# Kernel optimization log

Hardware: AMD Instinct MI355X
Metric: run time of the kernel (lower is better)

## Reference

```python
import jax, jax.numpy as jnp
import numpy as np

N_HEADS = 2


def setup_inputs() -> dict:
    key = jax.random.key(0)
    ks = jax.random.split(key, 12)
    B, S, d, g = 4096, 32, 512, 512
    sp = (1.0 / np.sqrt(d))
    sg = (1.0 / np.sqrt(g))
    return {
        "source": jax.random.normal(ks[0], (B, d), jnp.float32),
        "gene": jax.random.normal(ks[1], (B, S, g), jnp.float32),
        "neighbors_padding_mask": jax.random.bernoulli(ks[2], 0.3, (B, S)),
        "mask_n": jax.random.uniform(ks[3], (B, 1), jnp.float32),
        "Wq": jax.random.normal(ks[4], (d, d), jnp.float32) * sp,
        "bq": jax.random.normal(ks[5], (d,), jnp.float32) * 0.02,
        "Wk": jax.random.normal(ks[6], (d, g), jnp.float32) * sg,
        "bk": jax.random.normal(ks[7], (d,), jnp.float32) * 0.02,
        "Wv": jax.random.normal(ks[8], (d, g), jnp.float32) * sg,
        "bv": jax.random.normal(ks[9], (d,), jnp.float32) * 0.02,
        "Wout": jax.random.normal(ks[10], (d, d), jnp.float32) * sp,
        "bout": jax.random.normal(ks[11], (d,), jnp.float32) * 0.02,
    }


def reference(source, gene, neighbors_padding_mask, mask_n,
              Wq, bq, Wk, bk, Wv, bv, Wout, bout):
    # attention_node.forward: 1-query masked MHA over S temporal neighbors.
    B, S, _ = gene.shape
    d = source.shape[1]
    H = N_HEADS
    hd = d // H

    # rows where every neighbor is padded -> unmask slot 0 (torch in-place fix)
    invalid = jnp.all(neighbors_padding_mask, axis=1, keepdims=True)      # [B,1]
    mask = neighbors_padding_mask.at[:, 0].set(
        jnp.where(invalid[:, 0], False, neighbors_padding_mask[:, 0]))

    # separate q/k/v projections (kdim=vdim=n_gene != embed_dim)
    q = (source @ Wq.T + bq) * (hd ** -0.5)                               # [B,d]
    k = gene @ Wk.T + bk                                                  # [B,S,d]
    v = gene @ Wv.T + bv                                                  # [B,S,d]

    qh = q.reshape(B, H, hd)
    kh = k.reshape(B, S, H, hd)
    vh = v.reshape(B, S, H, hd)

    scores = jnp.einsum('bhd,bshd->bhs', qh, kh)                          # [B,H,S]
    scores = jnp.where(mask[:, None, :], -jnp.inf, scores)
    w = jax.nn.softmax(scores, axis=-1)                                   # [B,H,S]

    attn = jnp.einsum('bhs,bshd->bhd', w, vh).reshape(B, d)               # [B,d]
    attn_out = attn @ Wout.T + bout

    # zero rows with no valid neighbors, gate, residual
    attn_out = jnp.where(invalid, jnp.float32(0), attn_out)
    out = attn_out * mask_n + source                                      # [B,d]
    attn_weight = w.mean(axis=1)                                          # avg over heads, [B,S]
    return out, attn_weight
```

## Files before the change

### kernel.cpp

```cpp
#include <hip/hip_runtime.h>
#include <hip/hip_bf16.h>
#include <math.h>
#include <stdint.h>


#define NB 4096
#define SNB 32
#define DM 512

typedef __attribute__((ext_vector_type(8))) short bf16x8;
typedef __attribute__((ext_vector_type(4))) float f32x4;

__device__ __forceinline__ unsigned short f2bf(float f) {
    union { float f; unsigned int u; } v; v.f = f;
    unsigned int u = v.u;
    return (unsigned short)((u + 0x7FFFu + ((u >> 16) & 1u)) >> 16);
}
__device__ __forceinline__ float bf2f(unsigned short s) {
    union { unsigned int u; float f; } v; v.u = ((unsigned int)s) << 16;
    return v.f;
}

__global__ void k_detect(const unsigned int* __restrict__ m, int* __restrict__ mode) {
    __shared__ int fF, fH;
    if (threadIdx.x == 0) { fF = 0; fH = 0; }
    __syncthreads();
    int lf = 0, lh = 0;
    for (int i = threadIdx.x; i < 32768; i += blockDim.x) {
        unsigned int w = m[i];
        lf |= (w == 0x3F800000u);
        lh |= ((w & 0xFFFFFF00u) != 0u);
    }
    if (lf) atomicOr(&fF, 1);
    if (lh) atomicOr(&fH, 1);
    __syncthreads();
    if (threadIdx.x == 0) *mode = fF ? 2 : (fH ? 1 : 0);
}

__global__ void k_conv_src(const float* __restrict__ s, unsigned short* __restrict__ d) {
    int i = blockIdx.x * 256 + threadIdx.x;
    float4 v = ((const float4*)s)[i];
    ushort4 o;
    o.x = f2bf(v.x); o.y = f2bf(v.y); o.z = f2bf(v.z); o.w = f2bf(v.w);
    ((ushort4*)d)[i] = o;
}

__global__ __launch_bounds__(256) void k_precomp_cd(
    const float* __restrict__ Wq, const float* __restrict__ Wk,
    const float* __restrict__ Wv, const float* __restrict__ Wout,
    unsigned short* __restrict__ C, unsigned short* __restrict__ D)
{
    __shared__ float Aa[32][33];
    __shared__ float Bb[32][33];
    int bid = blockIdx.x;
    int t = threadIdx.x;
    float acc0 = 0.f, acc1 = 0.f, acc2 = 0.f, acc3 = 0.f;

    if (bid < 512) {
        int h = bid >> 8, rem = bid & 255;
        int j0 = (rem >> 4) << 5, m0 = (rem & 15) << 5;
        int ml = t & 31, jg = (t >> 5) << 2;
        for (int ic = 0; ic < 8; ic++) {
            int ib = h * 256 + ic * 32;
            for (int q = 0; q < 4; q++) {
                int idx = t + q * 256, rr = idx >> 5, cc = idx & 31;
                Aa[rr][cc] = Wk[(size_t)(ib + rr) * 512 + j0 + cc];
                Bb[rr][cc] = Wq[(size_t)(ib + rr) * 512 + m0 + cc];
            }
            __syncthreads();
            for (int i = 0; i < 32; i++) {
                float bqv = Bb[i][ml];
                acc0 += Aa[i][jg + 0] * bqv;
                acc1 += Aa[i][jg + 1] * bqv;
                acc2 += Aa[i][jg + 2] * bqv;
                acc3 += Aa[i][jg + 3] * bqv;
            }
            __syncthreads();
        }
        size_t p = (size_t)h * 512 + j0 + jg;
        C[(p + 0) * 512 + m0 + ml] = f2bf(0.0625f * acc0);
        C[(p + 1) * 512 + m0 + ml] = f2bf(0.0625f * acc1);
        C[(p + 2) * 512 + m0 + ml] = f2bf(0.0625f * acc2);
        C[(p + 3) * 512 + m0 + ml] = f2bf(0.0625f * acc3);
    } else {
        int bid2 = bid - 512;
        int h = bid2 >> 8, rem = bid2 & 255;
        int n0 = (rem >> 4) << 5, j0 = (rem & 15) << 5;
        int jl = t & 31, ng = (t >> 5) << 2;
        for (int ic = 0; ic < 8; ic++) {
            int ib = h * 256 + ic * 32;
            for (int q = 0; q < 4; q++) {
                int idx = t + q * 256, rr = idx >> 5, cc = idx & 31;
                Aa[rr][cc] = Wout[(size_t)(n0 + rr) * 512 + ib + cc];
                Bb[rr][cc] = Wv[(size_t)(ib + rr) * 512 + j0 + cc];
            }
            __syncthreads();
            for (int i = 0; i < 32; i++) {
                float bvv = Bb[i][jl];
                acc0 += Aa[ng + 0][i] * bvv;
                acc1 += Aa[ng + 1][i] * bvv;
                acc2 += Aa[ng + 2][i] * bvv;
                acc3 += Aa[ng + 3][i] * bvv;
            }
            __syncthreads();
        }
        size_t col = (size_t)h * 512 + j0 + jl;
        D[(size_t)(n0 + ng + 0) * 1024 + col] = f2bf(acc0);
        D[(size_t)(n0 + ng + 1) * 1024 + col] = f2bf(acc1);
        D[(size_t)(n0 + ng + 2) * 1024 + col] = f2bf(acc2);
        D[(size_t)(n0 + ng + 3) * 1024 + col] = f2bf(acc3);
    }
}

__global__ void k_precomp_vec(const float* __restrict__ Wk, const float* __restrict__ bq,
                              const float* __restrict__ Wout, const float* __restrict__ bv,
                              const float* __restrict__ bout,
                              float* __restrict__ cb, float* __restrict__ e)
{
    int t = blockIdx.x * 256 + threadIdx.x;
    if (t < 1024) {
        int h = t >> 9, j = t & 511;
        float a = 0.f;
        for (int i = 0; i < 256; i++) a += Wk[(size_t)(h * 256 + i) * 512 + j] * bq[h * 256 + i];
        cb[t] = 0.0625f * a;
    } else if (t < 1536) {
        int n = t - 1024;
        float a = bout[n];
        for (int i = 0; i < 512; i++) a += Wout[(size_t)n * 512 + i] * bv[i];
        e[n] = a;
    }
}

template <int EPI>
__global__ __launch_bounds__(256) void k_gemm_bt(
    const unsigned short* __restrict__ A, const unsigned short* __restrict__ Bt,
    void* __restrict__ outp, const float* __restrict__ bias,
    const float* __restrict__ gscale, const float* __restrict__ resid,
    int M, int N, int K)
{
    __shared__ __align__(16) unsigned short As[64 * 40];
    __shared__ __align__(16) unsigned short Bs[64 * 40];
    int nt = N >> 6;
    int m0 = ((int)blockIdx.x / nt) << 6;
    int n0 = ((int)blockIdx.x % nt) << 6;
    int t = threadIdx.x;
    int w = t >> 6, l = t & 63;
    int wm = (w >> 1) << 5, wn = (w & 1) << 5;
    int quad = l >> 4, lm = l & 15;

    f32x4 acc00 = {0.f, 0.f, 0.f, 0.f}, acc01 = {0.f, 0.f, 0.f, 0.f};
    f32x4 acc10 = {0.f, 0.f, 0.f, 0.f}, acc11 = {0.f, 0.f, 0.f, 0.f};

    int srow = t >> 2, spart = t & 3;
    const unsigned short* ag = A + (size_t)(m0 + srow) * K + spart * 8;
    const unsigned short* bg = Bt + (size_t)(n0 + srow) * K + spart * 8;
    unsigned short* asl = As + srow * 40 + spart * 8;
    unsigned short* bsl = Bs + srow * 40 + spart * 8;

    for (int k0 = 0; k0 < K; k0 += 32) {
        *(bf16x8*)asl = *(const bf16x8*)ag;
        *(bf16x8*)bsl = *(const bf16x8*)bg;
        ag += 32; bg += 32;
        __syncthreads();
        bf16x8 a0 = *(const bf16x8*)(As + (wm + lm) * 40 + quad * 8);
        bf16x8 a1 = *(const bf16x8*)(As + (wm + 16 + lm) * 40 + quad * 8);
        bf16x8 b0 = *(const bf16x8*)(Bs + (wn + lm) * 40 + quad * 8);
        bf16x8 b1 = *(const bf16x8*)(Bs + (wn + 16 + lm) * 40 + quad * 8);
        acc00 = __builtin_amdgcn_mfma_f32_16x16x32_bf16(a0, b0, acc00, 0, 0, 0);
        acc01 = __builtin_amdgcn_mfma_f32_16x16x32_bf16(a0, b1, acc01, 0, 0, 0);
        acc10 = __builtin_amdgcn_mfma_f32_16x16x32_bf16(a1, b0, acc10, 0, 0, 0);
        acc11 = __builtin_amdgcn_mfma_f32_16x16x32_bf16(a1, b1, acc11, 0, 0, 0);
        __syncthreads();
    }
    f32x4 accs[2][2] = {{acc00, acc01}, {acc10, acc11}};
    for (int ms = 0; ms < 2; ms++) {
        for (int ns = 0; ns < 2; ns++) {
            int n = n0 + wn + ns * 16 + lm;
            float bval = bias[n];
            for (int r = 0; r < 4; r++) {
                int m = m0 + wm + ms * 16 + quad * 4 + r;
                float v = accs[ms][ns][r] + bval;
                if (EPI == 0) {
                    ((unsigned short*)outp)[(size_t)m * N + n] = f2bf(v);
                } else {
                    ((float*)outp)[(size_t)m * N + n] =
                        v * gscale[m] + resid[(size_t)m * N + n];
                }
            }
        }
    }
}

__global__ __launch_bounds__(256) void k_attn(
    const float* __restrict__ gene, const unsigned short* __restrict__ QKb,
    const void* __restrict__ maskbuf, const int* __restrict__ modep,
    const float* __restrict__ mask_n,
    unsigned short* __restrict__ G, float* __restrict__ gscale,
    float* __restrict__ aw_out)
{
    __shared__ __align__(16) unsigned short glb[32 * 520];
    __shared__ __align__(16) unsigned short qka[16 * 520];
    __shared__ __align__(16) float sp[4 * 64];
    __shared__ __align__(16) float wls[64];
    __shared__ int msk_s[32];
    __shared__ int inv_s;

    int b = blockIdx.x, t = threadIdx.x;

    const float4* gp = (const float4*)(gene + (size_t)b * (SNB * DM));
    for (int it = 0; it < 8; it++) {
        float4 v0 = gp[t * 2 + it * 512];
        float4 v1 = gp[t * 2 + 1 + it * 512];
        int s = (t >> 6) + it * 4;
        int col = (t & 63) * 8;
        bf16x8 pk;
        pk[0] = (short)f2bf(v0.x); pk[1] = (short)f2bf(v0.y);
        pk[2] = (short)f2bf(v0.z); pk[3] = (short)f2bf(v0.w);
        pk[4] = (short)f2bf(v1.x); pk[5] = (short)f2bf(v1.y);
        pk[6] = (short)f2bf(v1.z); pk[7] = (short)f2bf(v1.w);
        *(bf16x8*)(glb + s * 520 + col) = pk;
    }
    {
        int h = (t * 4) >> 9, j = (t * 4) & 511;
        *(ushort4*)(qka + h * 520 + j) = *(const ushort4*)(QKb + (size_t)b * 1024 + t * 4);
    }
    {
        unsigned long long* z = (unsigned long long*)(qka + 2 * 520);
        for (int i = t; i < 1820; i += 256) z[i] = 0ull;
    }
    int mode = *modep;
    if (t < 32) {
        size_t off = (size_t)b * 32 + t;
        int mv;
        if (mode == 1)      mv = ((const unsigned char*)maskbuf)[off] != 0;
        else if (mode == 2) mv = (((const float*)maskbuf)[off] != 0.0f);
        else                mv = (((const int*)maskbuf)[off] != 0);
        msk_s[t] = mv;
    }
    __syncthreads();

    if (t == 0) {
        int all = 1;
        for (int s = 0; s < 32; s++) all &= msk_s[s];
        inv_s = all;
        if (all) msk_s[0] = 0;
        gscale[b] = all ? 0.0f : mask_n[b];
    }

    {
        int w = t >> 6, l = t & 63, quad = l >> 4, lm = l & 15;
        f32x4 s0 = {0.f, 0.f, 0.f, 0.f}, s1 = {0.f, 0.f, 0.f, 0.f};
        int kb = w * 128;
#pragma unroll
        for (int kk = 0; kk < 4; kk++) {
            int k0 = kb + kk * 32;
            bf16x8 af = *(const bf16x8*)(qka + lm * 520 + k0 + quad * 8);
            bf16x8 b0 = *(const bf16x8*)(glb + lm * 520 + k0 + quad * 8);
            bf16x8 b1 = *(const bf16x8*)(glb + (16 + lm) * 520 + k0 + quad * 8);
            s0 = __builtin_amdgcn_mfma_f32_16x16x32_bf16(af, b0, s0, 0, 0, 0);
            s1 = __builtin_amdgcn_mfma_f32_16x16x32_bf16(af, b1, s1, 0, 0, 0);
        }
        if (quad == 0) {
            sp[w * 64 + lm] = s0[0];
            sp[w * 64 + 32 + lm] = s0[1];
            sp[w * 64 + 16 + lm] = s1[0];
            sp[w * 64 + 48 + lm] = s1[1];
        }
    }
    __syncthreads();

    if (t < 64) {
        int s = t & 31;
        float v = sp[t] + sp[64 + t] + sp[128 + t] + sp[192 + t];
        int mk = msk_s[s];
        float vm = mk ? -1e30f : v;
        for (int off = 16; off > 0; off >>= 1) vm = fmaxf(vm, __shfl_xor(vm, off, 64));
        float ex = mk ? 0.0f : __expf(v - vm);
        float sm = ex;
        for (int off = 16; off > 0; off >>= 1) sm += __shfl_xor(sm, off, 64);
        wls[t] = ex / sm;
    }
    __syncthreads();

    if (t < 32) aw_out[(size_t)b * 32 + t] = 0.5f * (wls[t] + wls[32 + t]);

    {
        int h = t >> 7, jg = (t & 127) << 2;
        float a0 = 0.f, a1 = 0.f, a2 = 0.f, a3 = 0.f;
        const float* wrow = wls + h * 32;
        for (int s4 = 0; s4 < 8; s4++) {
            float4 wv = *(const float4*)(wrow + s4 * 4);
#pragma unroll
            for (int si = 0; si < 4; si++) {
                int s = s4 * 4 + si;
                ushort4 gv = *(const ushort4*)(glb + s * 520 + jg);
                float wq = (si == 0) ? wv.x : (si == 1) ? wv.y : (si == 2) ? wv.z : wv.w;
                a0 += wq * bf2f(gv.x); a1 += wq * bf2f(gv.y);
                a2 += wq * bf2f(gv.z); a3 += wq * bf2f(gv.w);
            }
        }
        ushort4 ov;
        ov.x = f2bf(a0); ov.y = f2bf(a1); ov.z = f2bf(a2); ov.w = f2bf(a3);
        *(ushort4*)(G + (size_t)b * 1024 + h * 512 + jg) = ov;
    }
}

extern "C" void kernel_launch(void* const* d_in, const int* in_sizes, int n_in,
                              void* d_out, int out_size, void* d_ws, size_t ws_size,
                              hipStream_t stream)
{
    const float* src   = (const float*)d_in[0];
    const float* gene  = (const float*)d_in[1];
    const void*  mask  = d_in[2];
    const float* maskn = (const float*)d_in[3];
    const float* Wq    = (const float*)d_in[4];
    const float* bq    = (const float*)d_in[5];
    const float* Wk    = (const float*)d_in[6];
    const float* Wv    = (const float*)d_in[8];
    const float* bv    = (const float*)d_in[9];
    const float* Wout  = (const float*)d_in[10];
    const float* bout  = (const float*)d_in[11];

    float* out = (float*)d_out;
    float* aw  = out + (size_t)NB * DM;

    char* ws = (char*)d_ws;
    size_t off = 0;
    auto alloc = [&](size_t bytes) -> void* {
        void* p = ws + off;
        off = (off + bytes + 255) & ~((size_t)255);
        return p;
    };
    int* mode            = (int*)alloc(4);
    unsigned short* srcb = (unsigned short*)alloc((size_t)NB * DM * 2);
    unsigned short* Cb   = (unsigned short*)alloc((size_t)1024 * 512 * 2);
    unsigned short* Db   = (unsigned short*)alloc((size_t)512 * 1024 * 2);
    float* cb            = (float*)alloc(1024 * 4);
    float* ev            = (float*)alloc(512 * 4);
    unsigned short* QKb  = (unsigned short*)alloc((size_t)NB * 1024 * 2);
    unsigned short* G    = (unsigned short*)alloc((size_t)NB * 1024 * 2);
    float* gs            = (float*)alloc((size_t)NB * 4);

    k_detect<<<1, 256, 0, stream>>>((const unsigned int*)mask, mode);
    k_conv_src<<<(NB * DM / 4) / 256, 256, 0, stream>>>(src, srcb);
    k_precomp_cd<<<1024, 256, 0, stream>>>(Wq, Wk, Wv, Wout, Cb, Db);
    k_precomp_vec<<<6, 256, 0, stream>>>(Wk, bq, Wout, bv, bout, cb, ev);
    k_gemm_bt<0><<<(4096 / 64) * (1024 / 64), 256, 0, stream>>>(
        srcb, Cb, QKb, cb, nullptr, nullptr, 4096, 1024, 512);
    k_attn<<<NB, 256, 0, stream>>>(gene, QKb, mask, mode, maskn, G, gs, aw);
    k_gemm_bt<1><<<(4096 / 64) * (512 / 64), 256, 0, stream>>>(
        G, Db, out, ev, gs, src, 4096, 512, 1024);
}
```

Baseline: 520.3 us.

## Move weight-product precompute to MFMA GEMM and merge prep kernels

New measurement: 461.4 us. 1.13x faster.

```diff
diff --git a/kernel.cpp b/kernel.cpp
--- a/kernel.cpp
+++ b/kernel.cpp
@@ -21,114 +21,155 @@
     return v.f;
 }
 
-__global__ void k_detect(const unsigned int* __restrict__ m, int* __restrict__ mode) {
+__global__ __launch_bounds__(256) void k_prep(
+    const float* __restrict__ src, const float* __restrict__ Wq,
+    const float* __restrict__ bq, const float* __restrict__ Wk,
+    const float* __restrict__ Wv, const float* __restrict__ Wout,
+    const float* __restrict__ bv, const float* __restrict__ bout,
+    const unsigned int* __restrict__ maskw,
+    unsigned short* __restrict__ srcb, unsigned short* __restrict__ WkT,
+    unsigned short* __restrict__ WqT, unsigned short* __restrict__ WvT,
+    unsigned short* __restrict__ WoutB,
+    float* __restrict__ cb, float* __restrict__ e, int* __restrict__ mode)
+{
+    __shared__ float tile[32][33];
     __shared__ int fF, fH;
-    if (threadIdx.x == 0) { fF = 0; fH = 0; }
-    __syncthreads();
-    int lf = 0, lh = 0;
-    for (int i = threadIdx.x; i < 32768; i += blockDim.x) {
-        unsigned int w = m[i];
-        lf |= (w == 0x3F800000u);
-        lh |= ((w & 0xFFFFFF00u) != 0u);
-    }
-    if (lf) atomicOr(&fF, 1);
-    if (lh) atomicOr(&fH, 1);
-    __syncthreads();
-    if (threadIdx.x == 0) *mode = fF ? 2 : (fH ? 1 : 0);
-}
-
-__global__ void k_conv_src(const float* __restrict__ s, unsigned short* __restrict__ d) {
-    int i = blockIdx.x * 256 + threadIdx.x;
-    float4 v = ((const float4*)s)[i];
-    ushort4 o;
-    o.x = f2bf(v.x); o.y = f2bf(v.y); o.z = f2bf(v.z); o.w = f2bf(v.w);
-    ((ushort4*)d)[i] = o;
-}
-
-__global__ __launch_bounds__(256) void k_precomp_cd(
-    const float* __restrict__ Wq, const float* __restrict__ Wk,
-    const float* __restrict__ Wv, const float* __restrict__ Wout,
+    int bid = blockIdx.x, t = threadIdx.x;
+
+    if (bid == 0) {
+        if (t == 0) { fF = 0; fH = 0; }
+        __syncthreads();
+        int lf = 0, lh = 0;
+        for (int i = t; i < 32768; i += 256) {
+            unsigned int w = maskw[i];
+            lf |= (w == 0x3F800000u);
+            lh |= ((w & 0xFFFFFF00u) != 0u);
+        }
+        if (lf) atomicOr(&fF, 1);
+        if (lh) atomicOr(&fH, 1);
+        __syncthreads();
+        if (t == 0) *mode = fF ? 2 : (fH ? 1 : 0);
+        return;
+    }
+    if (bid <= 4) {
+        int idx = (bid - 1) * 256 + t;
+        int h = idx >> 9, j = idx & 511;
+        float a = 0.f;
+        for (int i = 0; i < 256; i++)
+            a += Wk[(size_t)(h * 256 + i) * 512 + j] * bq[h * 256 + i];
+        cb[idx] = 0.0625f * a;
+        return;
+    }
+    if (bid <= 6) {
+        int n = (bid - 5) * 256 + t;
+        const float4* wr = (const float4*)(Wout + (size_t)n * 512);
+        const float4* bv4 = (const float4*)bv;
+        float a = bout[n];
+        for (int q = 0; q < 128; q++) {
+            float4 wv = wr[q], vv = bv4[q];
+            a += wv.x * vv.x + wv.y * vv.y + wv.z * vv.z + wv.w * vv.w;
+        }
+        e[n] = a;
+        return;
+    }
+    if (bid < 775) {
+        const float* sm; unsigned short* dst; float scale; int tt;
+        if (bid < 263)      { tt = bid - 7;   sm = Wk; dst = WkT; scale = 0.0625f; }
+        else if (bid < 519) { tt = bid - 263; sm = Wv; dst = WvT; scale = 1.0f; }
+        else                { tt = bid - 519; sm = Wq; dst = WqT; scale = 1.0f; }
+        int i0 = (tt >> 4) << 5, j0 = (tt & 15) << 5;
+        int r = t >> 3, c4 = (t & 7) << 2;
+        float4 v = *(const float4*)(sm + (size_t)(i0 + r) * 512 + j0 + c4);
+        tile[r][c4 + 0] = v.x; tile[r][c4 + 1] = v.y;
+        tile[r][c4 + 2] = v.z; tile[r][c4 + 3] = v.w;
+        __syncthreads();
+        int jj = t >> 3, ig = (t & 7) << 2;
+        int h = i0 >> 8, ib = i0 & 255;
+        ushort4 o;
+        o.x = f2bf(tile[ig + 0][jj] * scale);
+        o.y = f2bf(tile[ig + 1][jj] * scale);
+        o.z = f2bf(tile[ig + 2][jj] * scale);
+        o.w = f2bf(tile[ig + 3][jj] * scale);
+        *(ushort4*)(dst + (size_t)h * 131072 + (size_t)(j0 + jj) * 256 + ib + ig) = o;
+        return;
+    }
+    if (bid < 807) {
+        int base = (bid - 775) * 2048;
+        for (int q = 0; q < 8; q++) {
+            int idx = base + q * 256 + t;
+            float4 v = ((const float4*)Wout)[idx];
+            ushort4 o;
+            o.x = f2bf(v.x); o.y = f2bf(v.y); o.z = f2bf(v.z); o.w = f2bf(v.w);
+            ((ushort4*)WoutB)[idx] = o;
+        }
+        return;
+    }
+    {
+        int base = (bid - 807) * 2048;
+        for (int q = 0; q < 8; q++) {
+            int idx = base + q * 256 + t;
+            float4 v = ((const float4*)src)[idx];
+            ushort4 o;
+            o.x = f2bf(v.x); o.y = f2bf(v.y); o.z = f2bf(v.z); o.w = f2bf(v.w);
+            ((ushort4*)srcb)[idx] = o;
+        }
+    }
+}
+
+__global__ __launch_bounds__(256) void k_cd(
+    const unsigned short* __restrict__ WkT, const unsigned short* __restrict__ WqT,
+    const unsigned short* __restrict__ WoutB, const unsigned short* __restrict__ WvT,
     unsigned short* __restrict__ C, unsigned short* __restrict__ D)
 {
-    __shared__ float Aa[32][33];
-    __shared__ float Bb[32][33];
-    int bid = blockIdx.x;
-    int t = threadIdx.x;
-    float acc0 = 0.f, acc1 = 0.f, acc2 = 0.f, acc3 = 0.f;
-
-    if (bid < 512) {
-        int h = bid >> 8, rem = bid & 255;
-        int j0 = (rem >> 4) << 5, m0 = (rem & 15) << 5;
-        int ml = t & 31, jg = (t >> 5) << 2;
-        for (int ic = 0; ic < 8; ic++) {
-            int ib = h * 256 + ic * 32;
-            for (int q = 0; q < 4; q++) {
-                int idx = t + q * 256, rr = idx >> 5, cc = idx & 31;
-                Aa[rr][cc] = Wk[(size_t)(ib + rr) * 512 + j0 + cc];
-                Bb[rr][cc] = Wq[(size_t)(ib + rr) * 512 + m0 + cc];
-            }
-            __syncthreads();
-            for (int i = 0; i < 32; i++) {
-                float bqv = Bb[i][ml];
-                acc0 += Aa[i][jg + 0] * bqv;
-                acc1 += Aa[i][jg + 1] * bqv;
-                acc2 += Aa[i][jg + 2] * bqv;
-                acc3 += Aa[i][jg + 3] * bqv;
-            }
-            __syncthreads();
-        }
-        size_t p = (size_t)h * 512 + j0 + jg;
-        C[(p + 0) * 512 + m0 + ml] = f2bf(0.0625f * acc0);
-        C[(p + 1) * 512 + m0 + ml] = f2bf(0.0625f * acc1);
-        C[(p + 2) * 512 + m0 + ml] = f2bf(0.0625f * acc2);
-        C[(p + 3) * 512 + m0 + ml] = f2bf(0.0625f * acc3);
+    __shared__ __align__(16) unsigned short As[64 * 40];
+    __shared__ __align__(16) unsigned short Bs[64 * 40];
+    int bid = blockIdx.x, t = threadIdx.x;
+    const unsigned short *A, *Bt;
+    unsigned short* outp;
+    int lda, ldb, ldo;
+    if (bid < 128) {
+        int m0 = (bid >> 3) << 6, n0 = (bid & 7) << 6, h = m0 >> 9;
+        A = WkT + (size_t)m0 * 256; lda = 256;
+        Bt = WqT + (size_t)h * 131072 + (size_t)n0 * 256; ldb = 256;
+        outp = C + (size_t)m0 * 512 + n0; ldo = 512;
     } else {
-        int bid2 = bid - 512;
-        int h = bid2 >> 8, rem = bid2 & 255;
-        int n0 = (rem >> 4) << 5, j0 = (rem & 15) << 5;
-        int jl = t & 31, ng = (t >> 5) << 2;
-        for (int ic = 0; ic < 8; ic++) {
-            int ib = h * 256 + ic * 32;
-            for (int q = 0; q < 4; q++) {
-                int idx = t + q * 256, rr = idx >> 5, cc = idx & 31;
-                Aa[rr][cc] = Wout[(size_t)(n0 + rr) * 512 + ib + cc];
-                Bb[rr][cc] = Wv[(size_t)(ib + rr) * 512 + j0 + cc];
-            }
-            __syncthreads();
-            for (int i = 0; i < 32; i++) {
-                float bvv = Bb[i][jl];
-                acc0 += Aa[ng + 0][i] * bvv;
-                acc1 += Aa[ng + 1][i] * bvv;
-                acc2 += Aa[ng + 2][i] * bvv;
-                acc3 += Aa[ng + 3][i] * bvv;
-            }
-            __syncthreads();
-        }
-        size_t col = (size_t)h * 512 + j0 + jl;
-        D[(size_t)(n0 + ng + 0) * 1024 + col] = f2bf(acc0);
-        D[(size_t)(n0 + ng + 1) * 1024 + col] = f2bf(acc1);
-        D[(size_t)(n0 + ng + 2) * 1024 + col] = f2bf(acc2);
-        D[(size_t)(n0 + ng + 3) * 1024 + col] = f2bf(acc3);
-    }
-}
-
-__global__ void k_precomp_vec(const float* __restrict__ Wk, const float* __restrict__ bq,
-                              const float* __restrict__ Wout, const float* __restrict__ bv,
-                              const float* __restrict__ bout,
-                              float* __restrict__ cb, float* __restrict__ e)
-{
-    int t = blockIdx.x * 256 + threadIdx.x;
-    if (t < 1024) {
-        int h = t >> 9, j = t & 511;
-        float a = 0.f;
-        for (int i = 0; i < 256; i++) a += Wk[(size_t)(h * 256 + i) * 512 + j] * bq[h * 256 + i];
-        cb[t] = 0.0625f * a;
-    } else if (t < 1536) {
-        int n = t - 1024;
-        float a = bout[n];
-        for (int i = 0; i < 512; i++) a += Wout[(size_t)n * 512 + i] * bv[i];
-        e[n] = a;
-    }
+        int b2 = bid - 128;
+        int m0 = (b2 >> 4) << 6, n0 = (b2 & 15) << 6, h = n0 >> 9;
+        A = WoutB + (size_t)m0 * 512 + h * 256; lda = 512;
+        Bt = WvT + (size_t)n0 * 256; ldb = 256;
+        outp = D + (size_t)m0 * 1024 + n0; ldo = 1024;
+    }
+    int w = t >> 6, l = t & 63;
+    int wm = (w >> 1) << 5, wn = (w & 1) << 5;
+    int quad = l >> 4, lm = l & 15;
+    f32x4 acc00 = {0.f,0.f,0.f,0.f}, acc01 = {0.f,0.f,0.f,0.f};
+    f32x4 acc10 = {0.f,0.f,0.f,0.f}, acc11 = {0.f,0.f,0.f,0.f};
+    int srow = t >> 2, spart = t & 3;
+    const unsigned short* ag = A + (size_t)srow * lda + spart * 8;
+    const unsigned short* bg = Bt + (size_t)srow * ldb + spart * 8;
+    unsigned short* asl = As + srow * 40 + spart * 8;
+    unsigned short* bsl = Bs + srow * 40 + spart * 8;
+    for (int k0 = 0; k0 < 256; k0 += 32) {
+        *(bf16x8*)asl = *(const bf16x8*)ag;
+        *(bf16x8*)bsl = *(const bf16x8*)bg;
+        ag += 32; bg += 32;
+        __syncthreads();
+        bf16x8 a0 = *(const bf16x8*)(As + (wm + lm) * 40 + quad * 8);
+        bf16x8 a1 = *(const bf16x8*)(As + (wm + 16 + lm) * 40 + quad * 8);
+        bf16x8 b0 = *(const bf16x8*)(Bs + (wn + lm) * 40 + quad * 8);
+        bf16x8 b1 = *(const bf16x8*)(Bs + (wn + 16 + lm) * 40 + quad * 8);
+        acc00 = __builtin_amdgcn_mfma_f32_16x16x32_bf16(a0, b0, acc00, 0, 0, 0);
+        acc01 = __builtin_amdgcn_mfma_f32_16x16x32_bf16(a0, b1, acc01, 0, 0, 0);
+        acc10 = __builtin_amdgcn_mfma_f32_16x16x32_bf16(a1, b0, acc10, 0, 0, 0);
+        acc11 = __builtin_amdgcn_mfma_f32_16x16x32_bf16(a1, b1, acc11, 0, 0, 0);
+        __syncthreads();
+    }
+    f32x4 accs[2][2] = {{acc00, acc01}, {acc10, acc11}};
+    for (int ms = 0; ms < 2; ms++)
+        for (int ns = 0; ns < 2; ns++)
+            for (int r = 0; r < 4; r++)
+                outp[(size_t)(wm + ms * 16 + quad * 4 + r) * ldo + wn + ns * 16 + lm] =
+                    f2bf(accs[ms][ns][r]);
 }
 
 template <int EPI>
@@ -148,8 +189,8 @@
     int wm = (w >> 1) << 5, wn = (w & 1) << 5;
     int quad = l >> 4, lm = l & 15;
 
-    f32x4 acc00 = {0.f, 0.f, 0.f, 0.f}, acc01 = {0.f, 0.f, 0.f, 0.f};
-    f32x4 acc10 = {0.f, 0.f, 0.f, 0.f}, acc11 = {0.f, 0.f, 0.f, 0.f};
+    f32x4 acc00 = {0.f,0.f,0.f,0.f}, acc01 = {0.f,0.f,0.f,0.f};
+    f32x4 acc10 = {0.f,0.f,0.f,0.f}, acc11 = {0.f,0.f,0.f,0.f};
 
     int srow = t >> 2, spart = t & 3;
     const unsigned short* ag = A + (size_t)(m0 + srow) * K + spart * 8;
@@ -199,13 +240,23 @@
     float* __restrict__ aw_out)
 {
     __shared__ __align__(16) unsigned short glb[32 * 520];
-    __shared__ __align__(16) unsigned short qka[16 * 520];
     __shared__ __align__(16) float sp[4 * 64];
     __shared__ __align__(16) float wls[64];
     __shared__ int msk_s[32];
-    __shared__ int inv_s;
 
     int b = blockIdx.x, t = threadIdx.x;
+    int w = t >> 6, l = t & 63, quad = l >> 4, lm = l & 15;
+
+    bf16x8 af[4];
+    {
+        const unsigned short* qp = QKb + (size_t)b * 1024 + (size_t)lm * 512
+                                 + w * 128 + quad * 8;
+#pragma unroll
+        for (int kk = 0; kk < 4; kk++) {
+            bf16x8 z = {0,0,0,0,0,0,0,0};
+            af[kk] = (lm < 2) ? *(const bf16x8*)(qp + kk * 32) : z;
+        }
+    }
 
     const float4* gp = (const float4*)(gene + (size_t)b * (SNB * DM));
     for (int it = 0; it < 8; it++) {
@@ -220,21 +271,13 @@
         pk[6] = (short)f2bf(v1.z); pk[7] = (short)f2bf(v1.w);
         *(bf16x8*)(glb + s * 520 + col) = pk;
     }
-    {
-        int h = (t * 4) >> 9, j = (t * 4) & 511;
-        *(ushort4*)(qka + h * 520 + j) = *(const ushort4*)(QKb + (size_t)b * 1024 + t * 4);
-    }
-    {
-        unsigned long long* z = (unsigned long long*)(qka + 2 * 520);
-        for (int i = t; i < 1820; i += 256) z[i] = 0ull;
-    }
     int mode = *modep;
     if (t < 32) {
-        size_t off = (size_t)b * 32 + t;
+        size_t moff = (size_t)b * 32 + t;
         int mv;
-        if (mode == 1)      mv = ((const unsigned char*)maskbuf)[off] != 0;
-        else if (mode == 2) mv = (((const float*)maskbuf)[off] != 0.0f);
-        else                mv = (((const int*)maskbuf)[off] != 0);
+        if (mode == 1)      mv = ((const unsigned char*)maskbuf)[moff] != 0;
+        else if (mode == 2) mv = (((const float*)maskbuf)[moff] != 0.0f);
+        else                mv = (((const int*)maskbuf)[moff] != 0);
         msk_s[t] = mv;
     }
     __syncthreads();
@@ -242,23 +285,20 @@
     if (t == 0) {
         int all = 1;
         for (int s = 0; s < 32; s++) all &= msk_s[s];
-        inv_s = all;
         if (all) msk_s[0] = 0;
         gscale[b] = all ? 0.0f : mask_n[b];
     }
 
     {
-        int w = t >> 6, l = t & 63, quad = l >> 4, lm = l & 15;
-        f32x4 s0 = {0.f, 0.f, 0.f, 0.f}, s1 = {0.f, 0.f, 0.f, 0.f};
+        f32x4 s0 = {0.f,0.f,0.f,0.f}, s1 = {0.f,0.f,0.f,0.f};
         int kb = w * 128;
 #pragma unroll
         for (int kk = 0; kk < 4; kk++) {
             int k0 = kb + kk * 32;
-            bf16x8 af = *(const bf16x8*)(qka + lm * 520 + k0 + quad * 8);
             bf16x8 b0 = *(const bf16x8*)(glb + lm * 520 + k0 + quad * 8);
             bf16x8 b1 = *(const bf16x8*)(glb + (16 + lm) * 520 + k0 + quad * 8);
-            s0 = __builtin_amdgcn_mfma_f32_16x16x32_bf16(af, b0, s0, 0, 0, 0);
-            s1 = __builtin_amdgcn_mfma_f32_16x16x32_bf16(af, b1, s1, 0, 0, 0);
+            s0 = __builtin_amdgcn_mfma_f32_16x16x32_bf16(af[kk], b0, s0, 0, 0, 0);
+            s1 = __builtin_amdgcn_mfma_f32_16x16x32_bf16(af[kk], b1, s1, 0, 0, 0);
         }
         if (quad == 0) {
             sp[w * 64 + lm] = s0[0];
@@ -333,6 +373,10 @@
     };
     int* mode            = (int*)alloc(4);
     unsigned short* srcb = (unsigned short*)alloc((size_t)NB * DM * 2);
+    unsigned short* WkT  = (unsigned short*)alloc((size_t)1024 * 256 * 2);
+    unsigned short* WqT  = (unsigned short*)alloc((size_t)1024 * 256 * 2);
+    unsigned short* WvT  = (unsigned short*)alloc((size_t)1024 * 256 * 2);
+    unsigned short* WoB  = (unsigned short*)alloc((size_t)512 * 512 * 2);
     unsigned short* Cb   = (unsigned short*)alloc((size_t)1024 * 512 * 2);
     unsigned short* Db   = (unsigned short*)alloc((size_t)512 * 1024 * 2);
     float* cb            = (float*)alloc(1024 * 4);
@@ -341,10 +385,10 @@
     unsigned short* G    = (unsigned short*)alloc((size_t)NB * 1024 * 2);
     float* gs            = (float*)alloc((size_t)NB * 4);
 
-    k_detect<<<1, 256, 0, stream>>>((const unsigned int*)mask, mode);
-    k_conv_src<<<(NB * DM / 4) / 256, 256, 0, stream>>>(src, srcb);
-    k_precomp_cd<<<1024, 256, 0, stream>>>(Wq, Wk, Wv, Wout, Cb, Db);
-    k_precomp_vec<<<6, 256, 0, stream>>>(Wk, bq, Wout, bv, bout, cb, ev);
+    k_prep<<<1063, 256, 0, stream>>>(src, Wq, bq, Wk, Wv, Wout, bv, bout,
+                                     (const unsigned int*)mask,
+                                     srcb, WkT, WqT, WvT, WoB, cb, ev, mode);
+    k_cd<<<256, 256, 0, stream>>>(WkT, WqT, WoB, WvT, Cb, Db);
     k_gemm_bt<0><<<(4096 / 64) * (1024 / 64), 256, 0, stream>>>(
         srcb, Cb, QKb, cb, nullptr, nullptr, 4096, 1024, 512);
     k_attn<<<NB, 256, 0, stream>>>(gene, QKb, mask, mode, maskn, G, gs, aw);
```
